# Kernel optimization log

Measured on AMD Instinct MI355X. Metric: run time of the kernel, lower is better.

## Reference

```python
import jax, jax.numpy as jnp
import numpy as np

S, D_MODEL, H, D_K, D_V = 2048, 1024, 16, 64, 64


def setup_inputs() -> dict:
    key = jax.random.key(0)
    ks = jax.random.split(key, 10)
    sd = 0.02
    return {
        "embeddings": jax.random.normal(ks[0], (S, D_MODEL), dtype=jnp.float32),
        # per-head projection weights (torch Linear: y = x @ W.T + b; here stored as [h, d_in, d_out])
        "Wq": jax.random.normal(ks[1], (H, D_MODEL, D_K), dtype=jnp.float32) * sd,
        "bq": jax.random.normal(ks[2], (H, D_K), dtype=jnp.float32) * sd,
        "Wk": jax.random.normal(ks[3], (H, D_MODEL, D_K), dtype=jnp.float32) * sd,
        "bk": jax.random.normal(ks[4], (H, D_K), dtype=jnp.float32) * sd,
        "Wv": jax.random.normal(ks[5], (H, D_MODEL, D_V), dtype=jnp.float32) * sd,
        "bv": jax.random.normal(ks[6], (H, D_V), dtype=jnp.float32) * sd,
        "Wo": jax.random.normal(ks[7], (H * D_V, D_MODEL), dtype=jnp.float32) * sd,
        "bo": jax.random.normal(ks[8], (D_MODEL,), dtype=jnp.float32) * sd,
    }


def reference(embeddings, Wq, bq, Wk, bk, Wv, bv, Wo, bo):
    # Batched equivalent of the per-head Python loop of ScaledDotProductAttention layers.
    # q,k: [h, s, d_k]; v: [h, s, d_v]
    q = jnp.einsum('sd,hdk->hsk', embeddings, Wq) + bq[:, None, :]
    k = jnp.einsum('sd,hdk->hsk', embeddings, Wk) + bk[:, None, :]
    v = jnp.einsum('sd,hdv->hsv', embeddings, Wv) + bv[:, None, :]
    scale = jnp.asarray(1.0 / np.sqrt(q.shape[-1]), q.dtype)
    scores = jnp.einsum('hsk,htk->hst', q, k) * scale  # [h, s, s]
    attn = jax.nn.softmax(scores, axis=-1)
    heads = jnp.einsum('hst,htv->hsv', attn, v)  # [h, s, d_v]
    # torch.cat(results, dim=1): head outputs concatenated along feature dim -> [s, h*d_v]
    concat = jnp.transpose(heads, (1, 0, 2)).reshape(embeddings.shape[0], -1)
    return concat @ Wo + bo
```

## Files before the change

kernel.cpp:

```cpp
#include <hip/hip_runtime.h>
#include <hip/hip_bf16.h>

typedef unsigned short u16;
typedef __attribute__((ext_vector_type(8))) short bf16x8;
typedef __attribute__((ext_vector_type(4))) float f32x4;

#define S_LEN 2048
#define NH 16

__device__ __forceinline__ u16 f2bf(float x) {
  union { float f; unsigned u; } v; v.f = x;
  unsigned r = v.u + 0x7fffu + ((v.u >> 16) & 1u);
  return (u16)(r >> 16);
}

__device__ __forceinline__ unsigned cvtpk_bf16(float lo, float hi) {
  unsigned w;
  asm("v_cvt_pk_bf16_f32 %0, %1, %2" : "=v"(w) : "v"(lo), "v"(hi));
  return w;
}

__device__ __forceinline__ void async16(const void* g, void* l) {
  __builtin_amdgcn_global_load_lds(
      (const __attribute__((address_space(1))) unsigned int*)g,
      (__attribute__((address_space(3))) unsigned int*)l, 16, 0, 0);
}

__device__ __forceinline__ f32x4 mfma16(bf16x8 a, bf16x8 b, f32x4 c) {
  return __builtin_amdgcn_mfma_f32_16x16x32_bf16(a, b, c, 0, 0, 0);
}

#define QSCALE (0.125f * 1.44269504089f)

__global__ __launch_bounds__(256) void convert_kernel(
    const float* __restrict__ emb, const float* __restrict__ Wq,
    const float* __restrict__ Wk, const float* __restrict__ Wv,
    const float* __restrict__ bq, const float* __restrict__ bk,
    const float* __restrict__ bv, const float* __restrict__ Wo,
    u16* __restrict__ emb_bf, u16* __restrict__ wqkv_t,
    u16* __restrict__ wo_t, float* __restrict__ bqkv) {
  __shared__ float lds[64][65];
  const int b = blockIdx.x, tid = threadIdx.x;
  if (b < 2048) {
    int i = b * 1024 + tid * 4;
    float4 v = *(const float4*)(emb + i);
    ushort4 o = {f2bf(v.x), f2bf(v.y), f2bf(v.z), f2bf(v.w)};
    *(ushort4*)(emb_bf + i) = o;
    return;
  }
  if (b < 2816) {
    int tt = b - 2048;
    int kind = tt >> 8;
    int rem = tt & 255;
    int h = rem >> 4, k0 = (rem & 15) << 6;
    const float* W = (kind == 0) ? Wq : ((kind == 1) ? Wk : Wv);
    const float* src = W + ((size_t)h * 1024 + k0) * 64;
#pragma unroll
    for (int rr = 0; rr < 4; ++rr) {
      int k = rr * 16 + (tid >> 4);
      int d4 = (tid & 15) << 2;
      float4 v = *(const float4*)(src + (size_t)k * 64 + d4);
      lds[k][d4] = v.x; lds[k][d4 + 1] = v.y;
      lds[k][d4 + 2] = v.z; lds[k][d4 + 3] = v.w;
    }
    __syncthreads();
    float scale = (kind == 0) ? QSCALE : 1.f;
#pragma unroll
    for (int p = 0; p < 2; ++p) {
      int d = p * 32 + (tid >> 3);
      int kb = (tid & 7) << 3;
      bf16x8 o;
#pragma unroll
      for (int j = 0; j < 8; ++j) o[j] = (short)f2bf(lds[kb + j][d] * scale);
      *(bf16x8*)(wqkv_t + (size_t)(kind * 1024 + h * 64 + d) * 1024 + k0 + kb) = o;
    }
    return;
  }
  if (b < 3072) {
    int tt = b - 2816;
    int k0 = (tt >> 4) << 6, n0 = (tt & 15) << 6;
#pragma unroll
    for (int rr = 0; rr < 4; ++rr) {
      int k = rr * 16 + (tid >> 4);
      int n4 = (tid & 15) << 2;
      float4 v = *(const float4*)(Wo + (size_t)(k0 + k) * 1024 + n0 + n4);
      lds[k][n4] = v.x; lds[k][n4 + 1] = v.y;
      lds[k][n4 + 2] = v.z; lds[k][n4 + 3] = v.w;
    }
    __syncthreads();
#pragma unroll
    for (int p = 0; p < 2; ++p) {
      int nrel = p * 32 + (tid >> 3);
      int kb = (tid & 7) << 3;
      bf16x8 o;
#pragma unroll
      for (int j = 0; j < 8; ++j) o[j] = (short)f2bf(lds[kb + j][nrel]);
      *(bf16x8*)(wo_t + (size_t)(n0 + nrel) * 1024 + k0 + kb) = o;
    }
    return;
  }
  for (int i = tid; i < 3072; i += 256) {
    int kind = i >> 10, hd = i & 1023;
    const float* bb = (kind == 0) ? bq : ((kind == 1) ? bk : bv);
    float v = bb[hd];
    bqkv[i] = (kind == 0) ? v * QSCALE : v;
  }
}

template <int WM, int WN, int FM, int FN, int BK, bool OUT_BF16>
__global__ __launch_bounds__(WM * WN * 64) void gemm_kernel(
    const u16* __restrict__ A, const u16* __restrict__ BT,
    const float* __restrict__ bias, void* __restrict__ Cout, int M, int N,
    int K) {
  constexpr int BM = WM * FM * 16, BN = WN * FN * 16, T = WM * WN * 64;
  constexpr int RB = BK * 2;
  __shared__ u16 lds[2][(BM + BN) * BK];
  const int tid = threadIdx.x;
  const int lane = tid & 63, wave = tid >> 6;
  const int wr = wave / WN, wc = wave % WN;
  const int m0 = blockIdx.x * BM, n0 = blockIdx.y * BN;
  const int r = lane & 15, g = lane >> 4;
  const f32x4 fzero = {0.f, 0.f, 0.f, 0.f};
  f32x4 acc[FM][FN];
#pragma unroll
  for (int i = 0; i < FM; ++i)
#pragma unroll
    for (int j = 0; j < FN; ++j) acc[i][j] = fzero;

  constexpr int LA = (BM * RB) / (T * 16);
  constexpr int LB = (BN * RB) / (T * 16);

  auto stage = [&](int kt, int buf) {
    int k0 = kt * BK;
#pragma unroll
    for (int i = 0; i < LA; ++i) {
      int flat = i * T * 16 + tid * 16;
      int row = flat / RB, colb = flat % RB;
      async16((const char*)A + ((size_t)(m0 + row) * K + k0) * 2 + colb,
              (char*)lds[buf] + i * T * 16 + wave * 1024);
    }
#pragma unroll
    for (int i = 0; i < LB; ++i) {
      int flat = i * T * 16 + tid * 16;
      int row = flat / RB, colb = flat % RB;
      async16((const char*)BT + ((size_t)(n0 + row) * K + k0) * 2 + colb,
              (char*)lds[buf] + BM * RB + i * T * 16 + wave * 1024);
    }
  };

  stage(0, 0);
  asm volatile("s_waitcnt vmcnt(0)" ::: "memory");
  __syncthreads();

  const int NT = K / BK;
  for (int kt = 0; kt < NT; ++kt) {
    int cur = kt & 1;
    if (kt + 1 < NT) stage(kt + 1, cur ^ 1);
    const u16* Al = lds[cur];
    const u16* Bl = Al + BM * BK;
#pragma unroll
    for (int kk = 0; kk < BK / 32; ++kk) {
      bf16x8 af[FM], bfr[FN];
#pragma unroll
      for (int i = 0; i < FM; ++i)
        af[i] = *(const bf16x8*)&Al[(wr * FM * 16 + i * 16 + r) * BK + kk * 32 + g * 8];
#pragma unroll
      for (int j = 0; j < FN; ++j)
        bfr[j] = *(const bf16x8*)&Bl[(wc * FN * 16 + j * 16 + r) * BK + kk * 32 + g * 8];
#pragma unroll
      for (int i = 0; i < FM; ++i)
#pragma unroll
        for (int j = 0; j < FN; ++j)
          acc[i][j] = mfma16(af[i], bfr[j], acc[i][j]);
    }
    asm volatile("s_waitcnt vmcnt(0)" ::: "memory");
    __syncthreads();
  }

#pragma unroll
  for (int i = 0; i < FM; ++i)
#pragma unroll
    for (int j = 0; j < FN; ++j)
#pragma unroll
      for (int e = 0; e < 4; ++e) {
        int row = m0 + wr * FM * 16 + i * 16 + g * 4 + e;
        int col = n0 + wc * FN * 16 + j * 16 + r;
        float v = acc[i][j][e] + bias[col];
        if constexpr (OUT_BF16)
          ((u16*)Cout)[(size_t)row * N + col] = f2bf(v);
        else
          ((float*)Cout)[(size_t)row * N + col] = v;
      }
}

__global__ __launch_bounds__(256) void vtrans_kernel(const u16* __restrict__ qkv,
                                                     u16* __restrict__ vt) {
  __shared__ unsigned lds[64][65];
  const int b = blockIdx.x, tid = threadIdx.x;
  const int h = b >> 5, s0 = (b & 31) << 6;
#pragma unroll
  for (int p = 0; p < 2; ++p) {
    int srow = p * 32 + (tid >> 3);
    int dblk = (tid & 7) << 3;
    bf16x8 v = *(const bf16x8*)(qkv + (size_t)(s0 + srow) * 3072 + 2048 + h * 64 + dblk);
#pragma unroll
    for (int j = 0; j < 8; ++j) lds[srow][dblk + j] = (u16)v[j];
  }
  __syncthreads();
#pragma unroll
  for (int p = 0; p < 2; ++p) {
    int d = p * 32 + (tid >> 3);
    int sb = (tid & 7) << 3;
    bf16x8 w;
#pragma unroll
    for (int j = 0; j < 8; ++j) w[j] = (short)(u16)lds[sb + j][d];
    *(bf16x8*)(vt + (size_t)h * 131072 + (size_t)d * 2048 + s0 + sb) = w;
  }
}

__global__ __launch_bounds__(512) void attn_kernel(const u16* __restrict__ qkv,
                                                   const u16* __restrict__ vt,
                                                   u16* __restrict__ concat) {
  __shared__ __align__(16) char smem[81920];
  const int tid = threadIdx.x;
  const int lane = tid & 63, wave = tid >> 6;
  const int qg = wave >> 1, kvw = wave & 1;
  const int h = blockIdx.y;
  const int q0 = blockIdx.x * 64 + qg * 16;
  const int r = lane & 15, g = lane >> 4;
  const f32x4 fzero = {0.f, 0.f, 0.f, 0.f};
  char* Pw = smem + 65536 + wave * 2048;

  bf16x8 aq[2];
#pragma unroll
  for (int kk = 0; kk < 2; ++kk)
    aq[kk] = *(const bf16x8*)&qkv[(size_t)(q0 + r) * 3072 + h * 64 + kk * 32 + g * 8];

  f32x4 acc[4];
#pragma unroll
  for (int nt = 0; nt < 4; ++nt) acc[nt] = fzero;
  float rs = 0.f;

  auto stage = [&](int step) {
    int par = step & 1;
    int t0 = step * 128;
#pragma unroll
    for (int i = 0; i < 2; ++i) {
      int flat = i * 8192 + tid * 16;
      int row = flat >> 7;
      int blk = ((flat >> 4) & 7) ^ (row & 7);
      const char* srcK = (const char*)qkv +
                         ((size_t)(t0 + row) * 3072 + 1024 + h * 64) * 2 + blk * 16;
      async16(srcK, smem + par * 16384 + i * 8192 + wave * 1024);
      int c = row >> 6, d = row & 63;
      const char* srcV = (const char*)vt +
                         ((size_t)h * 131072 + (size_t)d * 2048 + t0 + c * 64) * 2 + blk * 16;
      async16(srcV, smem + 32768 + par * 16384 + i * 8192 + wave * 1024);
    }
  };

  stage(0);
  asm volatile("s_waitcnt vmcnt(0)" ::: "memory");
  __syncthreads();

  for (int step = 0; step < 16; ++step) {
    if (step + 1 < 16) stage(step + 1);
    const int par = step & 1;
    const char* Kb = smem + par * 16384 + kvw * 8192;
    const char* Vb = smem + 32768 + par * 16384 + kvw * 8192;

    f32x4 sv[4];
    __builtin_amdgcn_s_setprio(1);
#pragma unroll
    for (int nt = 0; nt < 4; ++nt) {
      f32x4 a = fzero;
#pragma unroll
      for (int kk = 0; kk < 2; ++kk) {
        int row = nt * 16 + r;
        const bf16x8 bk = *(const bf16x8*)(Kb + row * 128 +
                                           ((((kk << 2) | g) ^ (row & 7)) << 4));
        a = mfma16(bk, aq[kk], a);
      }
      sv[nt] = a;
    }
    __builtin_amdgcn_s_setprio(0);

#pragma unroll
    for (int nt = 0; nt < 4; ++nt) {
      float p0 = exp2f(sv[nt][0]), p1 = exp2f(sv[nt][1]);
      float p2 = exp2f(sv[nt][2]), p3 = exp2f(sv[nt][3]);
      rs += (p0 + p1) + (p2 + p3);
      uint2 w = {cvtpk_bf16(p0, p1), cvtpk_bf16(p2, p3)};
      int off = (r * 128 + nt * 32 + g * 8) ^ ((r & 7) << 4);
      *(uint2*)(Pw + off) = w;
    }

    asm volatile("s_waitcnt lgkmcnt(0)" ::: "memory");
    __builtin_amdgcn_sched_barrier(0);
    bf16x8 pa[2];
#pragma unroll
    for (int tc = 0; tc < 2; ++tc)
      pa[tc] = *(const bf16x8*)(Pw + ((r * 128 + tc * 64 + g * 16) ^ ((r & 7) << 4)));
    __builtin_amdgcn_s_setprio(1);
#pragma unroll
    for (int nt = 0; nt < 4; ++nt)
#pragma unroll
      for (int tc = 0; tc < 2; ++tc) {
        int d = (nt << 4) | r;
        const bf16x8 bv = *(const bf16x8*)(Vb + d * 128 +
                                           ((((tc << 2) | g) ^ (d & 7)) << 4));
        acc[nt] = mfma16(pa[tc], bv, acc[nt]);
      }
    __builtin_amdgcn_s_setprio(0);
    asm volatile("s_waitcnt vmcnt(0)" ::: "memory");
    __syncthreads();
  }

  rs += __shfl_xor(rs, 16, 64);
  rs += __shfl_xor(rs, 32, 64);

  float* Ox = (float*)smem;
  float* Lx = (float*)(smem + 64 * 65 * 4);
  if (kvw == 1) {
#pragma unroll
    for (int nt = 0; nt < 4; ++nt)
#pragma unroll
      for (int e = 0; e < 4; ++e)
        Ox[(qg * 16 + (g << 2) + e) * 65 + (nt << 4) + r] = acc[nt][e];
    if (g == 0) Lx[qg * 16 + r] = rs;
  }
  __syncthreads();
  if (kvw == 0) {
    float inv[4];
#pragma unroll
    for (int e = 0; e < 4; ++e) {
      float own = __shfl(rs, (g << 2) | e, 64);
      inv[e] = 1.f / (own + Lx[qg * 16 + (g << 2) + e]);
    }
#pragma unroll
    for (int nt = 0; nt < 4; ++nt)
#pragma unroll
      for (int e = 0; e < 4; ++e) {
        float o = acc[nt][e] + Ox[(qg * 16 + (g << 2) + e) * 65 + (nt << 4) + r];
        concat[(size_t)(q0 + (g << 2) + e) * 1024 + h * 64 + (nt << 4) + r] =
            f2bf(o * inv[e]);
      }
  }
}

extern "C" void kernel_launch(void* const* d_in, const int* in_sizes, int n_in,
                              void* d_out, int out_size, void* d_ws,
                              size_t ws_size, hipStream_t stream) {
  (void)in_sizes; (void)n_in; (void)out_size; (void)ws_size;
  const float* emb = (const float*)d_in[0];
  const float* Wq = (const float*)d_in[1];
  const float* bq = (const float*)d_in[2];
  const float* Wk = (const float*)d_in[3];
  const float* bk = (const float*)d_in[4];
  const float* Wv = (const float*)d_in[5];
  const float* bv = (const float*)d_in[6];
  const float* Wo = (const float*)d_in[7];
  const float* bo = (const float*)d_in[8];

  char* ws = (char*)d_ws;
  u16* emb_bf  = (u16*)(ws + 0);
  u16* wqkv_t  = (u16*)(ws + 4194304);
  u16* wo_t    = (u16*)(ws + 10485760);
  float* bqkv  = (float*)(ws + 12582912);
  u16* qkv     = (u16*)(ws + 12595200);
  u16* vt      = (u16*)(ws + 25178112);
  u16* concat  = (u16*)(ws + 29372416);

  convert_kernel<<<3073, 256, 0, stream>>>(emb, Wq, Wk, Wv, bq, bk, bv, Wo,
                                           emb_bf, wqkv_t, wo_t, bqkv);
  gemm_kernel<2, 2, 4, 2, 64, true><<<dim3(16, 48), 256, 0, stream>>>(
      emb_bf, wqkv_t, bqkv, qkv, 2048, 3072, 1024);
  vtrans_kernel<<<512, 256, 0, stream>>>(qkv, vt);
  attn_kernel<<<dim3(32, 16), 512, 0, stream>>>(qkv, vt, concat);
  gemm_kernel<2, 2, 2, 2, 64, false><<<dim3(32, 16), 256, 0, stream>>>(
      concat, wo_t, bo, d_out, 2048, 1024, 1024);
}
```

Measured before the change: 84.86 us.

## Fuse V transpose into QKV GEMM epilogue; double query rows per attention wave

```diff
diff --git a/kernel.cpp b/kernel.cpp
--- a/kernel.cpp
+++ b/kernel.cpp
@@ -107,11 +107,11 @@
   }
 }
 
-template <int WM, int WN, int FM, int FN, int BK, bool OUT_BF16>
+template <int WM, int WN, int FM, int FN, int BK, bool OUT_BF16, bool VT_SPLIT>
 __global__ __launch_bounds__(WM * WN * 64) void gemm_kernel(
     const u16* __restrict__ A, const u16* __restrict__ BT,
-    const float* __restrict__ bias, void* __restrict__ Cout, int M, int N,
-    int K) {
+    const float* __restrict__ bias, void* __restrict__ Cout,
+    u16* __restrict__ vt, int M, int N, int K) {
   constexpr int BM = WM * FM * 16, BN = WN * FN * 16, T = WM * WN * 64;
   constexpr int RB = BK * 2;
   __shared__ u16 lds[2][(BM + BN) * BK];
@@ -177,6 +177,24 @@
     __syncthreads();
   }
 
+  if constexpr (VT_SPLIT) {
+    if (n0 >= 2048) {
+      int h = (n0 - 2048) >> 6;
+#pragma unroll
+      for (int i = 0; i < FM; ++i)
+#pragma unroll
+        for (int j = 0; j < FN; ++j) {
+          int d = wc * FN * 16 + j * 16 + r;
+          int s0 = m0 + wr * FM * 16 + i * 16 + g * 4;
+          float bval = bias[n0 + (d & 63)];
+          ushort4 o = {f2bf(acc[i][j][0] + bval), f2bf(acc[i][j][1] + bval),
+                       f2bf(acc[i][j][2] + bval), f2bf(acc[i][j][3] + bval)};
+          *(ushort4*)(vt + (size_t)h * 131072 + (size_t)d * 2048 + s0) = o;
+        }
+      return;
+    }
+  }
+
 #pragma unroll
   for (int i = 0; i < FM; ++i)
 #pragma unroll
@@ -193,32 +211,7 @@
       }
 }
 
-__global__ __launch_bounds__(256) void vtrans_kernel(const u16* __restrict__ qkv,
-                                                     u16* __restrict__ vt) {
-  __shared__ unsigned lds[64][65];
-  const int b = blockIdx.x, tid = threadIdx.x;
-  const int h = b >> 5, s0 = (b & 31) << 6;
-#pragma unroll
-  for (int p = 0; p < 2; ++p) {
-    int srow = p * 32 + (tid >> 3);
-    int dblk = (tid & 7) << 3;
-    bf16x8 v = *(const bf16x8*)(qkv + (size_t)(s0 + srow) * 3072 + 2048 + h * 64 + dblk);
-#pragma unroll
-    for (int j = 0; j < 8; ++j) lds[srow][dblk + j] = (u16)v[j];
-  }
-  __syncthreads();
-#pragma unroll
-  for (int p = 0; p < 2; ++p) {
-    int d = p * 32 + (tid >> 3);
-    int sb = (tid & 7) << 3;
-    bf16x8 w;
-#pragma unroll
-    for (int j = 0; j < 8; ++j) w[j] = (short)(u16)lds[sb + j][d];
-    *(bf16x8*)(vt + (size_t)h * 131072 + (size_t)d * 2048 + s0 + sb) = w;
-  }
-}
-
-__global__ __launch_bounds__(512) void attn_kernel(const u16* __restrict__ qkv,
+__global__ __launch_bounds__(256) void attn_kernel(const u16* __restrict__ qkv,
                                                    const u16* __restrict__ vt,
                                                    u16* __restrict__ concat) {
   __shared__ __align__(16) char smem[81920];
@@ -226,36 +219,41 @@
   const int lane = tid & 63, wave = tid >> 6;
   const int qg = wave >> 1, kvw = wave & 1;
   const int h = blockIdx.y;
-  const int q0 = blockIdx.x * 64 + qg * 16;
+  const int q0w = blockIdx.x * 64 + qg * 32;
   const int r = lane & 15, g = lane >> 4;
   const f32x4 fzero = {0.f, 0.f, 0.f, 0.f};
-  char* Pw = smem + 65536 + wave * 2048;
-
-  bf16x8 aq[2];
-#pragma unroll
-  for (int kk = 0; kk < 2; ++kk)
-    aq[kk] = *(const bf16x8*)&qkv[(size_t)(q0 + r) * 3072 + h * 64 + kk * 32 + g * 8];
-
-  f32x4 acc[4];
-#pragma unroll
-  for (int nt = 0; nt < 4; ++nt) acc[nt] = fzero;
-  float rs = 0.f;
+  char* Pw = smem + 65536 + wave * 4096;
+
+  bf16x8 aq[2][2];
+#pragma unroll
+  for (int qi = 0; qi < 2; ++qi)
+#pragma unroll
+    for (int kk = 0; kk < 2; ++kk)
+      aq[qi][kk] = *(const bf16x8*)&qkv[(size_t)(q0w + qi * 16 + r) * 3072 +
+                                        h * 64 + kk * 32 + g * 8];
+
+  f32x4 acc[4][2];
+#pragma unroll
+  for (int nt = 0; nt < 4; ++nt)
+#pragma unroll
+    for (int qi = 0; qi < 2; ++qi) acc[nt][qi] = fzero;
+  float rs[2] = {0.f, 0.f};
 
   auto stage = [&](int step) {
     int par = step & 1;
     int t0 = step * 128;
 #pragma unroll
-    for (int i = 0; i < 2; ++i) {
-      int flat = i * 8192 + tid * 16;
+    for (int i = 0; i < 4; ++i) {
+      int flat = i * 4096 + tid * 16;
       int row = flat >> 7;
       int blk = ((flat >> 4) & 7) ^ (row & 7);
       const char* srcK = (const char*)qkv +
                          ((size_t)(t0 + row) * 3072 + 1024 + h * 64) * 2 + blk * 16;
-      async16(srcK, smem + par * 16384 + i * 8192 + wave * 1024);
+      async16(srcK, smem + par * 16384 + i * 4096 + wave * 1024);
       int c = row >> 6, d = row & 63;
       const char* srcV = (const char*)vt +
                          ((size_t)h * 131072 + (size_t)d * 2048 + t0 + c * 64) * 2 + blk * 16;
-      async16(srcV, smem + 32768 + par * 16384 + i * 8192 + wave * 1024);
+      async16(srcV, smem + 32768 + par * 16384 + i * 4096 + wave * 1024);
     }
   };
 
@@ -269,38 +267,46 @@
     const char* Kb = smem + par * 16384 + kvw * 8192;
     const char* Vb = smem + 32768 + par * 16384 + kvw * 8192;
 
-    f32x4 sv[4];
+    f32x4 sv[4][2];
     __builtin_amdgcn_s_setprio(1);
 #pragma unroll
     for (int nt = 0; nt < 4; ++nt) {
-      f32x4 a = fzero;
+      sv[nt][0] = fzero;
+      sv[nt][1] = fzero;
 #pragma unroll
       for (int kk = 0; kk < 2; ++kk) {
         int row = nt * 16 + r;
         const bf16x8 bk = *(const bf16x8*)(Kb + row * 128 +
                                            ((((kk << 2) | g) ^ (row & 7)) << 4));
-        a = mfma16(bk, aq[kk], a);
-      }
-      sv[nt] = a;
+        sv[nt][0] = mfma16(bk, aq[0][kk], sv[nt][0]);
+        sv[nt][1] = mfma16(bk, aq[1][kk], sv[nt][1]);
+      }
     }
     __builtin_amdgcn_s_setprio(0);
 
 #pragma unroll
-    for (int nt = 0; nt < 4; ++nt) {
-      float p0 = exp2f(sv[nt][0]), p1 = exp2f(sv[nt][1]);
-      float p2 = exp2f(sv[nt][2]), p3 = exp2f(sv[nt][3]);
-      rs += (p0 + p1) + (p2 + p3);
-      uint2 w = {cvtpk_bf16(p0, p1), cvtpk_bf16(p2, p3)};
-      int off = (r * 128 + nt * 32 + g * 8) ^ ((r & 7) << 4);
-      *(uint2*)(Pw + off) = w;
-    }
+    for (int nt = 0; nt < 4; ++nt)
+#pragma unroll
+      for (int qi = 0; qi < 2; ++qi) {
+        float p0 = exp2f(sv[nt][qi][0]), p1 = exp2f(sv[nt][qi][1]);
+        float p2 = exp2f(sv[nt][qi][2]), p3 = exp2f(sv[nt][qi][3]);
+        rs[qi] += (p0 + p1) + (p2 + p3);
+        uint2 w = {cvtpk_bf16(p0, p1), cvtpk_bf16(p2, p3)};
+        int q = qi * 16 + r;
+        int off = (q * 128 + nt * 32 + g * 8) ^ ((q & 7) << 4);
+        *(uint2*)(Pw + off) = w;
+      }
 
     asm volatile("s_waitcnt lgkmcnt(0)" ::: "memory");
     __builtin_amdgcn_sched_barrier(0);
-    bf16x8 pa[2];
-#pragma unroll
-    for (int tc = 0; tc < 2; ++tc)
-      pa[tc] = *(const bf16x8*)(Pw + ((r * 128 + tc * 64 + g * 16) ^ ((r & 7) << 4)));
+    bf16x8 pa[2][2];
+#pragma unroll
+    for (int qi = 0; qi < 2; ++qi)
+#pragma unroll
+      for (int tc = 0; tc < 2; ++tc) {
+        int q = qi * 16 + r;
+        pa[qi][tc] = *(const bf16x8*)(Pw + ((q * 128 + tc * 64 + g * 16) ^ ((q & 7) << 4)));
+      }
     __builtin_amdgcn_s_setprio(1);
 #pragma unroll
     for (int nt = 0; nt < 4; ++nt)
@@ -309,15 +315,19 @@
         int d = (nt << 4) | r;
         const bf16x8 bv = *(const bf16x8*)(Vb + d * 128 +
                                            ((((tc << 2) | g) ^ (d & 7)) << 4));
-        acc[nt] = mfma16(pa[tc], bv, acc[nt]);
+        acc[nt][0] = mfma16(pa[0][tc], bv, acc[nt][0]);
+        acc[nt][1] = mfma16(pa[1][tc], bv, acc[nt][1]);
       }
     __builtin_amdgcn_s_setprio(0);
     asm volatile("s_waitcnt vmcnt(0)" ::: "memory");
     __syncthreads();
   }
 
-  rs += __shfl_xor(rs, 16, 64);
-  rs += __shfl_xor(rs, 32, 64);
+#pragma unroll
+  for (int qi = 0; qi < 2; ++qi) {
+    rs[qi] += __shfl_xor(rs[qi], 16, 64);
+    rs[qi] += __shfl_xor(rs[qi], 32, 64);
+  }
 
   float* Ox = (float*)smem;
   float* Lx = (float*)(smem + 64 * 65 * 4);
@@ -325,26 +335,37 @@
 #pragma unroll
     for (int nt = 0; nt < 4; ++nt)
 #pragma unroll
-      for (int e = 0; e < 4; ++e)
-        Ox[(qg * 16 + (g << 2) + e) * 65 + (nt << 4) + r] = acc[nt][e];
-    if (g == 0) Lx[qg * 16 + r] = rs;
+      for (int qi = 0; qi < 2; ++qi)
+#pragma unroll
+        for (int e = 0; e < 4; ++e) {
+          int qb = qg * 32 + qi * 16 + (g << 2) + e;
+          Ox[qb * 65 + (nt << 4) + r] = acc[nt][qi][e];
+        }
+    if (g == 0) {
+      Lx[qg * 32 + r] = rs[0];
+      Lx[qg * 32 + 16 + r] = rs[1];
+    }
   }
   __syncthreads();
   if (kvw == 0) {
-    float inv[4];
-#pragma unroll
-    for (int e = 0; e < 4; ++e) {
-      float own = __shfl(rs, (g << 2) | e, 64);
-      inv[e] = 1.f / (own + Lx[qg * 16 + (g << 2) + e]);
-    }
-#pragma unroll
-    for (int nt = 0; nt < 4; ++nt)
+#pragma unroll
+    for (int qi = 0; qi < 2; ++qi) {
+      float inv[4];
 #pragma unroll
       for (int e = 0; e < 4; ++e) {
-        float o = acc[nt][e] + Ox[(qg * 16 + (g << 2) + e) * 65 + (nt << 4) + r];
-        concat[(size_t)(q0 + (g << 2) + e) * 1024 + h * 64 + (nt << 4) + r] =
-            f2bf(o * inv[e]);
-      }
+        float own = __shfl(rs[qi], (g << 2) | e, 64);
+        inv[e] = 1.f / (own + Lx[qg * 32 + qi * 16 + (g << 2) + e]);
+      }
+#pragma unroll
+      for (int nt = 0; nt < 4; ++nt)
+#pragma unroll
+        for (int e = 0; e < 4; ++e) {
+          int qb = qg * 32 + qi * 16 + (g << 2) + e;
+          float o = acc[nt][qi][e] + Ox[qb * 65 + (nt << 4) + r];
+          concat[(size_t)(blockIdx.x * 64 + qb) * 1024 + h * 64 + (nt << 4) + r] =
+              f2bf(o * inv[e]);
+        }
+    }
   }
 }
 
@@ -373,10 +394,9 @@
 
   convert_kernel<<<3073, 256, 0, stream>>>(emb, Wq, Wk, Wv, bq, bk, bv, Wo,
                                            emb_bf, wqkv_t, wo_t, bqkv);
-  gemm_kernel<2, 2, 4, 2, 64, true><<<dim3(16, 48), 256, 0, stream>>>(
-      emb_bf, wqkv_t, bqkv, qkv, 2048, 3072, 1024);
-  vtrans_kernel<<<512, 256, 0, stream>>>(qkv, vt);
-  attn_kernel<<<dim3(32, 16), 512, 0, stream>>>(qkv, vt, concat);
-  gemm_kernel<2, 2, 2, 2, 64, false><<<dim3(32, 16), 256, 0, stream>>>(
-      concat, wo_t, bo, d_out, 2048, 1024, 1024);
-}
+  gemm_kernel<2, 2, 4, 2, 64, true, true><<<dim3(16, 48), 256, 0, stream>>>(
+      emb_bf, wqkv_t, bqkv, qkv, vt, 2048, 3072, 1024);
+  attn_kernel<<<dim3(32, 16), 256, 0, stream>>>(qkv, vt, concat);
+  gemm_kernel<2, 2, 2, 2, 64, false, false><<<dim3(32, 16), 256, 0, stream>>>(
+      concat, wo_t, bo, d_out, nullptr, 2048, 1024, 1024);
+}
```

Result: no change. 86.01 us (+1.4%).

## Fuse V transpose and K packing into QKV GEMM epilogue, deepen pipelines

Applied to the files above, without the earlier changes.

```diff
diff --git a/kernel.cpp b/kernel.cpp
--- a/kernel.cpp
+++ b/kernel.cpp
@@ -20,10 +20,29 @@
   return w;
 }
 
+__device__ __forceinline__ float fexp2(float x) {
+#if __has_builtin(__builtin_amdgcn_exp2f)
+  return __builtin_amdgcn_exp2f(x);
+#else
+  float y;
+  asm volatile("v_exp_f32 %0, %1\n\ts_nop 0" : "=v"(y) : "v"(x));
+  return y;
+#endif
+}
+
 __device__ __forceinline__ void async16(const void* g, void* l) {
   __builtin_amdgcn_global_load_lds(
       (const __attribute__((address_space(1))) unsigned int*)g,
       (__attribute__((address_space(3))) unsigned int*)l, 16, 0, 0);
+}
+
+template <int N>
+__device__ __forceinline__ void vmwait() {
+  asm volatile("s_waitcnt vmcnt(%0)" ::"i"(N) : "memory");
+}
+__device__ __forceinline__ void wgbar() {
+  __builtin_amdgcn_s_barrier();
+  __builtin_amdgcn_sched_barrier(0);
 }
 
 __device__ __forceinline__ f32x4 mfma16(bf16x8 a, bf16x8 b, f32x4 c) {
@@ -107,14 +126,14 @@
   }
 }
 
-template <int WM, int WN, int FM, int FN, int BK, bool OUT_BF16>
+template <int WM, int WN, int FM, int FN, int BK, bool OUT_BF16, bool SPLIT>
 __global__ __launch_bounds__(WM * WN * 64) void gemm_kernel(
     const u16* __restrict__ A, const u16* __restrict__ BT,
-    const float* __restrict__ bias, void* __restrict__ Cout, int M, int N,
-    int K) {
+    const float* __restrict__ bias, void* __restrict__ Cout,
+    u16* __restrict__ kp, u16* __restrict__ vt, int M, int N, int K) {
   constexpr int BM = WM * FM * 16, BN = WN * FN * 16, T = WM * WN * 64;
   constexpr int RB = BK * 2;
-  __shared__ u16 lds[2][(BM + BN) * BK];
+  __shared__ u16 lds[3][(BM + BN) * BK];
   const int tid = threadIdx.x;
   const int lane = tid & 63, wave = tid >> 6;
   const int wr = wave / WN, wc = wave % WN;
@@ -129,6 +148,7 @@
 
   constexpr int LA = (BM * RB) / (T * 16);
   constexpr int LB = (BN * RB) / (T * 16);
+  constexpr int LPS = LA + LB;
 
   auto stage = [&](int kt, int buf) {
     int k0 = kt * BK;
@@ -148,15 +168,15 @@
     }
   };
 
+  const int NT = K / BK;
   stage(0, 0);
-  asm volatile("s_waitcnt vmcnt(0)" ::: "memory");
-  __syncthreads();
-
-  const int NT = K / BK;
+  stage(1, 1);
+  vmwait<LPS>();
+  wgbar();
+
   for (int kt = 0; kt < NT; ++kt) {
-    int cur = kt & 1;
-    if (kt + 1 < NT) stage(kt + 1, cur ^ 1);
-    const u16* Al = lds[cur];
+    if (kt + 2 < NT) stage(kt + 2, (kt + 2) % 3);
+    const u16* Al = lds[kt % 3];
     const u16* Bl = Al + BM * BK;
 #pragma unroll
     for (int kk = 0; kk < BK / 32; ++kk) {
@@ -173,8 +193,44 @@
         for (int j = 0; j < FN; ++j)
           acc[i][j] = mfma16(af[i], bfr[j], acc[i][j]);
     }
-    asm volatile("s_waitcnt vmcnt(0)" ::: "memory");
-    __syncthreads();
+    if (kt + 2 < NT) { vmwait<LPS>(); }
+    else if (kt + 1 < NT) { vmwait<0>(); }
+    if (kt + 1 < NT) wgbar();
+  }
+
+  if constexpr (SPLIT) {
+    if (n0 >= 2048) {
+      int h = (n0 - 2048) >> 6;
+#pragma unroll
+      for (int i = 0; i < FM; ++i)
+#pragma unroll
+        for (int j = 0; j < FN; ++j) {
+          int d = wc * FN * 16 + j * 16 + r;
+          int s0 = m0 + wr * FM * 16 + i * 16 + g * 4;
+          float bval = bias[n0 + d];
+          ushort4 o = {f2bf(acc[i][j][0] + bval), f2bf(acc[i][j][1] + bval),
+                       f2bf(acc[i][j][2] + bval), f2bf(acc[i][j][3] + bval)};
+          *(ushort4*)(vt + (size_t)h * 131072 + (size_t)(s0 >> 6) * 4096 +
+                      d * 64 + (s0 & 63)) = o;
+        }
+      return;
+    }
+    if (n0 >= 1024) {
+      int h = (n0 - 1024) >> 6;
+#pragma unroll
+      for (int i = 0; i < FM; ++i)
+#pragma unroll
+        for (int j = 0; j < FN; ++j) {
+          int d = wc * FN * 16 + j * 16 + r;
+          float bval = bias[n0 + d];
+#pragma unroll
+          for (int e = 0; e < 4; ++e) {
+            int row = m0 + wr * FM * 16 + i * 16 + g * 4 + e;
+            kp[((size_t)h * 2048 + row) * 64 + d] = f2bf(acc[i][j][e] + bval);
+          }
+        }
+      return;
+    }
   }
 
 #pragma unroll
@@ -193,140 +249,120 @@
       }
 }
 
-__global__ __launch_bounds__(256) void vtrans_kernel(const u16* __restrict__ qkv,
-                                                     u16* __restrict__ vt) {
-  __shared__ unsigned lds[64][65];
-  const int b = blockIdx.x, tid = threadIdx.x;
-  const int h = b >> 5, s0 = (b & 31) << 6;
-#pragma unroll
-  for (int p = 0; p < 2; ++p) {
-    int srow = p * 32 + (tid >> 3);
-    int dblk = (tid & 7) << 3;
-    bf16x8 v = *(const bf16x8*)(qkv + (size_t)(s0 + srow) * 3072 + 2048 + h * 64 + dblk);
-#pragma unroll
-    for (int j = 0; j < 8; ++j) lds[srow][dblk + j] = (u16)v[j];
-  }
-  __syncthreads();
-#pragma unroll
-  for (int p = 0; p < 2; ++p) {
-    int d = p * 32 + (tid >> 3);
-    int sb = (tid & 7) << 3;
-    bf16x8 w;
-#pragma unroll
-    for (int j = 0; j < 8; ++j) w[j] = (short)(u16)lds[sb + j][d];
-    *(bf16x8*)(vt + (size_t)h * 131072 + (size_t)d * 2048 + s0 + sb) = w;
-  }
-}
-
 __global__ __launch_bounds__(512) void attn_kernel(const u16* __restrict__ qkv,
+                                                   const u16* __restrict__ kp,
                                                    const u16* __restrict__ vt,
                                                    u16* __restrict__ concat) {
-  __shared__ __align__(16) char smem[81920];
+  __shared__ __align__(16) char smem[65536];
   const int tid = threadIdx.x;
   const int lane = tid & 63, wave = tid >> 6;
   const int qg = wave >> 1, kvw = wave & 1;
   const int h = blockIdx.y;
-  const int q0 = blockIdx.x * 64 + qg * 16;
+  const int q0w = blockIdx.x * 64 + qg * 16;
   const int r = lane & 15, g = lane >> 4;
+  const bool hi = (lane & 32) != 0;
+  const int sa0 = (((lane & 16) << 1) | r) << 2;
+  const int sa1 = sa0 + 64;
   const f32x4 fzero = {0.f, 0.f, 0.f, 0.f};
-  char* Pw = smem + 65536 + wave * 2048;
 
   bf16x8 aq[2];
 #pragma unroll
   for (int kk = 0; kk < 2; ++kk)
-    aq[kk] = *(const bf16x8*)&qkv[(size_t)(q0 + r) * 3072 + h * 64 + kk * 32 + g * 8];
+    aq[kk] = *(const bf16x8*)&qkv[(size_t)(q0w + r) * 3072 + h * 64 + kk * 32 + g * 8];
 
   f32x4 acc[4];
 #pragma unroll
   for (int nt = 0; nt < 4; ++nt) acc[nt] = fzero;
   float rs = 0.f;
 
+  const char* kbase = (const char*)kp + (size_t)h * 262144;
+  const char* vbase = (const char*)vt + (size_t)h * 262144;
+  const int flat = tid * 16;
+  const int srow = flat >> 7;
+  const int sflat = flat ^ ((srow & 7) << 4);
+
   auto stage = [&](int step) {
-    int par = step & 1;
-    int t0 = step * 128;
-#pragma unroll
-    for (int i = 0; i < 2; ++i) {
-      int flat = i * 8192 + tid * 16;
-      int row = flat >> 7;
-      int blk = ((flat >> 4) & 7) ^ (row & 7);
-      const char* srcK = (const char*)qkv +
-                         ((size_t)(t0 + row) * 3072 + 1024 + h * 64) * 2 + blk * 16;
-      async16(srcK, smem + par * 16384 + i * 8192 + wave * 1024);
-      int c = row >> 6, d = row & 63;
-      const char* srcV = (const char*)vt +
-                         ((size_t)h * 131072 + (size_t)d * 2048 + t0 + c * 64) * 2 + blk * 16;
-      async16(srcV, smem + 32768 + par * 16384 + i * 8192 + wave * 1024);
-    }
+    char* dst = smem + (step & 3) * 16384 + flat;
+    async16(kbase + (size_t)step * 8192 + sflat, dst);
+    async16(vbase + (size_t)step * 8192 + sflat, dst + 8192);
   };
 
-  stage(0);
-  asm volatile("s_waitcnt vmcnt(0)" ::: "memory");
-  __syncthreads();
-
-  for (int step = 0; step < 16; ++step) {
-    if (step + 1 < 16) stage(step + 1);
-    const int par = step & 1;
-    const char* Kb = smem + par * 16384 + kvw * 8192;
-    const char* Vb = smem + 32768 + par * 16384 + kvw * 8192;
-
-    f32x4 sv[4];
+  constexpr int NT = 32;
+  stage(0); stage(1); stage(2);
+  vmwait<4>();
+  wgbar();
+
+  for (int t = 0; t < NT; ++t) {
+    if (t + 3 < NT) stage(t + 3);
+    const char* Kb = smem + (t & 3) * 16384;
+    const char* Vb = Kb + 8192;
+
+    f32x4 sv[2];
     __builtin_amdgcn_s_setprio(1);
 #pragma unroll
-    for (int nt = 0; nt < 4; ++nt) {
-      f32x4 a = fzero;
+    for (int nt = 0; nt < 2; ++nt) {
+      sv[nt] = fzero;
+      int row = kvw * 32 + nt * 16 + r;
 #pragma unroll
       for (int kk = 0; kk < 2; ++kk) {
-        int row = nt * 16 + r;
         const bf16x8 bk = *(const bf16x8*)(Kb + row * 128 +
                                            ((((kk << 2) | g) ^ (row & 7)) << 4));
-        a = mfma16(bk, aq[kk], a);
+        sv[nt] = mfma16(bk, aq[kk], sv[nt]);
       }
-      sv[nt] = a;
     }
     __builtin_amdgcn_s_setprio(0);
 
+    int w_[2][2];
+#pragma unroll
+    for (int nt = 0; nt < 2; ++nt) {
+      float p0 = fexp2(sv[nt][0]), p1 = fexp2(sv[nt][1]);
+      float p2 = fexp2(sv[nt][2]), p3 = fexp2(sv[nt][3]);
+      rs += (p0 + p1) + (p2 + p3);
+      w_[nt][0] = (int)cvtpk_bf16(p0, p1);
+      w_[nt][1] = (int)cvtpk_bf16(p2, p3);
+    }
+
+    int a0 = __builtin_amdgcn_ds_bpermute(sa0, w_[0][0]);
+    int a1 = __builtin_amdgcn_ds_bpermute(sa0, w_[1][0]);
+    int b0 = __builtin_amdgcn_ds_bpermute(sa0, w_[0][1]);
+    int b1 = __builtin_amdgcn_ds_bpermute(sa0, w_[1][1]);
+    int c0 = __builtin_amdgcn_ds_bpermute(sa1, w_[0][0]);
+    int c1 = __builtin_amdgcn_ds_bpermute(sa1, w_[1][0]);
+    int d0 = __builtin_amdgcn_ds_bpermute(sa1, w_[0][1]);
+    int d1 = __builtin_amdgcn_ds_bpermute(sa1, w_[1][1]);
+    int4 u = {hi ? a1 : a0, hi ? b1 : b0, hi ? c1 : c0, hi ? d1 : d0};
+    bf16x8 pa = *(bf16x8*)&u;
+
+    __builtin_amdgcn_s_setprio(1);
 #pragma unroll
     for (int nt = 0; nt < 4; ++nt) {
-      float p0 = exp2f(sv[nt][0]), p1 = exp2f(sv[nt][1]);
-      float p2 = exp2f(sv[nt][2]), p3 = exp2f(sv[nt][3]);
-      rs += (p0 + p1) + (p2 + p3);
-      uint2 w = {cvtpk_bf16(p0, p1), cvtpk_bf16(p2, p3)};
-      int off = (r * 128 + nt * 32 + g * 8) ^ ((r & 7) << 4);
-      *(uint2*)(Pw + off) = w;
-    }
-
-    asm volatile("s_waitcnt lgkmcnt(0)" ::: "memory");
-    __builtin_amdgcn_sched_barrier(0);
-    bf16x8 pa[2];
-#pragma unroll
-    for (int tc = 0; tc < 2; ++tc)
-      pa[tc] = *(const bf16x8*)(Pw + ((r * 128 + tc * 64 + g * 16) ^ ((r & 7) << 4)));
-    __builtin_amdgcn_s_setprio(1);
-#pragma unroll
-    for (int nt = 0; nt < 4; ++nt)
-#pragma unroll
-      for (int tc = 0; tc < 2; ++tc) {
-        int d = (nt << 4) | r;
-        const bf16x8 bv = *(const bf16x8*)(Vb + d * 128 +
-                                           ((((tc << 2) | g) ^ (d & 7)) << 4));
-        acc[nt] = mfma16(pa[tc], bv, acc[nt]);
-      }
+      int d = nt * 16 + r;
+      const bf16x8 bv = *(const bf16x8*)(Vb + d * 128 +
+                                         ((((kvw << 2) | g) ^ (d & 7)) << 4));
+      acc[nt] = mfma16(pa, bv, acc[nt]);
+    }
     __builtin_amdgcn_s_setprio(0);
-    asm volatile("s_waitcnt vmcnt(0)" ::: "memory");
-    __syncthreads();
+
+    if (t + 3 < NT) { vmwait<4>(); }
+    else if (t + 2 < NT) { vmwait<2>(); }
+    else if (t + 1 < NT) { vmwait<0>(); }
+    if (t + 1 < NT) wgbar();
   }
 
   rs += __shfl_xor(rs, 16, 64);
   rs += __shfl_xor(rs, 32, 64);
 
+  __syncthreads();
   float* Ox = (float*)smem;
   float* Lx = (float*)(smem + 64 * 65 * 4);
   if (kvw == 1) {
 #pragma unroll
     for (int nt = 0; nt < 4; ++nt)
 #pragma unroll
-      for (int e = 0; e < 4; ++e)
-        Ox[(qg * 16 + (g << 2) + e) * 65 + (nt << 4) + r] = acc[nt][e];
+      for (int e = 0; e < 4; ++e) {
+        int qb = qg * 16 + (g << 2) + e;
+        Ox[qb * 65 + nt * 16 + r] = acc[nt][e];
+      }
     if (g == 0) Lx[qg * 16 + r] = rs;
   }
   __syncthreads();
@@ -334,16 +370,19 @@
     float inv[4];
 #pragma unroll
     for (int e = 0; e < 4; ++e) {
+      int qb = qg * 16 + (g << 2) + e;
       float own = __shfl(rs, (g << 2) | e, 64);
-      inv[e] = 1.f / (own + Lx[qg * 16 + (g << 2) + e]);
+      inv[e] = 1.f / (own + Lx[qb]);
     }
 #pragma unroll
     for (int nt = 0; nt < 4; ++nt)
 #pragma unroll
       for (int e = 0; e < 4; ++e) {
-        float o = acc[nt][e] + Ox[(qg * 16 + (g << 2) + e) * 65 + (nt << 4) + r];
-        concat[(size_t)(q0 + (g << 2) + e) * 1024 + h * 64 + (nt << 4) + r] =
-            f2bf(o * inv[e]);
+        int qb = qg * 16 + (g << 2) + e;
+        int d = nt * 16 + r;
+        float o = acc[nt][e] + Ox[qb * 65 + d];
+        concat[(size_t)(blockIdx.x * 64 + qg * 16 + (g << 2) + e) * 1024 +
+               h * 64 + d] = f2bf(o * inv[e]);
       }
   }
 }
@@ -370,13 +409,13 @@
   u16* qkv     = (u16*)(ws + 12595200);
   u16* vt      = (u16*)(ws + 25178112);
   u16* concat  = (u16*)(ws + 29372416);
+  u16* kpack   = (u16*)(ws + 33566720);
 
   convert_kernel<<<3073, 256, 0, stream>>>(emb, Wq, Wk, Wv, bq, bk, bv, Wo,
                                            emb_bf, wqkv_t, wo_t, bqkv);
-  gemm_kernel<2, 2, 4, 2, 64, true><<<dim3(16, 48), 256, 0, stream>>>(
-      emb_bf, wqkv_t, bqkv, qkv, 2048, 3072, 1024);
-  vtrans_kernel<<<512, 256, 0, stream>>>(qkv, vt);
-  attn_kernel<<<dim3(32, 16), 512, 0, stream>>>(qkv, vt, concat);
-  gemm_kernel<2, 2, 2, 2, 64, false><<<dim3(32, 16), 256, 0, stream>>>(
-      concat, wo_t, bo, d_out, 2048, 1024, 1024);
-}
+  gemm_kernel<2, 2, 4, 2, 64, true, true><<<dim3(16, 48), 256, 0, stream>>>(
+      emb_bf, wqkv_t, bqkv, qkv, kpack, vt, 2048, 3072, 1024);
+  attn_kernel<<<dim3(32, 16), 512, 0, stream>>>(qkv, kpack, vt, concat);
+  gemm_kernel<2, 2, 2, 2, 64, false, false><<<dim3(32, 16), 256, 0, stream>>>(
+      concat, wo_t, bo, d_out, nullptr, nullptr, 2048, 1024, 1024);
+}
```

New measurement: 90.41 us. 1.07x slower.
